# Performance work log

Measured on AMD Instinct MI355X. Metric: run time of the kernel, lower is better.

The kernel has to match this reference:

```python
import jax, jax.numpy as jnp
import numpy as np

B, T, D_MODEL, D_HIDDEN, MAX_SEQLEN = 4, 2048, 1024, 256, 2048


def setup_inputs() -> dict:
    key = jax.random.key(0)
    ks = jax.random.split(key, 8)
    s_in = 1.0 / np.sqrt(D_MODEL)
    s_out = 1.0 / np.sqrt(D_HIDDEN)
    # xavier_uniform bound for W_bias (fan_in = fan_out = MAX_SEQLEN)
    xb = np.sqrt(6.0 / (MAX_SEQLEN + MAX_SEQLEN))
    return {
        "q": jax.random.normal(ks[0], (B, T, D_MODEL), jnp.float32),
        "k": jax.random.normal(ks[1], (B, T, D_MODEL), jnp.float32),
        "v": jax.random.normal(ks[2], (B, T, D_MODEL), jnp.float32),
        "Wq": jax.random.normal(ks[3], (D_MODEL, D_HIDDEN), jnp.float32) * s_in,
        "Wk": jax.random.normal(ks[4], (D_MODEL, D_HIDDEN), jnp.float32) * s_in,
        "Wv": jax.random.normal(ks[5], (D_MODEL, D_HIDDEN), jnp.float32) * s_in,
        "Wo": jax.random.normal(ks[6], (D_HIDDEN, D_MODEL), jnp.float32) * s_out,
        "W_bias": jax.random.uniform(ks[7], (MAX_SEQLEN, MAX_SEQLEN), jnp.float32, -xb, xb),
    }


def reference(q, k, v, Wq, Wk, Wv, Wo, W_bias):
    Ti, Tj = q.shape[1], k.shape[1]
    Q = q @ Wq                      # [B,Ti,dh]
    K = k @ Wk                      # [B,Tj,dh]
    V = v @ Wv                      # [B,Tj,dh]
    pos_bias = W_bias[:Ti, :Tj][None]               # [1,Ti,Tj]
    # NOTE: source subtracts max over dim 0 (batch). For pos_bias that dim is 1,
    # so exp_pos_bias == exp(0) == ones -- reproduced faithfully here.
    max_key = jnp.max(K, axis=0, keepdims=True)      # [1,Tj,dh]
    max_pos_bias = jnp.max(pos_bias, axis=0, keepdims=True)
    exp_key = jnp.exp(K - max_key)                   # [B,Tj,dh]
    exp_pos_bias = jnp.exp(pos_bias - max_pos_bias)  # [1,Ti,Tj]
    num = jnp.einsum('ij,bjd->bid', exp_pos_bias[0], exp_key * V)  # [B,Ti,dh]
    den = jnp.einsum('ij,bjd->bid', exp_pos_bias[0], exp_key)      # [B,Ti,dh]
    Yt = jax.nn.sigmoid(Q) * num / den
    return Yt @ Wo                  # [B,Ti,d_model]
```

## Files before the change

kernel.cpp:

```cpp
#include <hip/hip_runtime.h>
#include <hip/hip_bf16.h>
#include <math.h>

#define B_   4
#define T_   2048
#define DM   1024
#define DH   256
#define M_   (B_*T_)

typedef __bf16 bf16;
typedef __attribute__((ext_vector_type(8))) __bf16 bf16x8;
typedef __attribute__((ext_vector_type(4))) float  f32x4;

#define LDT 72

__device__ inline float sigmoidf_(float x) { return 1.0f / (1.0f + __expf(-x)); }

__global__ void transpose_cvt(const float* __restrict__ in, bf16* __restrict__ out,
                              int R, int C) {
    __shared__ float tile[32][33];
    int c0 = blockIdx.x * 32, r0 = blockIdx.y * 32;
    int tx = threadIdx.x & 31, ty = threadIdx.x >> 5;
    #pragma unroll
    for (int i = ty; i < 32; i += 8)
        tile[i][tx] = in[(long)(r0 + i) * C + c0 + tx];
    __syncthreads();
    #pragma unroll
    for (int i = ty; i < 32; i += 8)
        out[(long)(c0 + i) * R + r0 + tx] = (bf16)tile[tx][i];
}

__global__ __launch_bounds__(256)
void gemm_proj(const float* __restrict__ qin, const float* __restrict__ kin,
               const float* __restrict__ vin,
               const bf16* __restrict__ Wq_t, const bf16* __restrict__ Wk_t,
               const bf16* __restrict__ Wv_t,
               bf16* __restrict__ Qb, bf16* __restrict__ Kb, bf16* __restrict__ Vb)
{
    __shared__ __align__(16) bf16 As[64][LDT];
    __shared__ __align__(16) bf16 Bs[64][LDT];

    const int z = blockIdx.z;
    const float* A  = (z == 0) ? qin  : (z == 1) ? kin  : vin;
    const bf16*  Wt = (z == 0) ? Wq_t : (z == 1) ? Wk_t : Wv_t;
    bf16*        C  = (z == 0) ? Qb   : (z == 1) ? Kb   : Vb;

    const int m0 = blockIdx.x * 64;
    const int n0 = blockIdx.y * 64;
    const int tid = threadIdx.x, lane = tid & 63, wave = tid >> 6;
    const int wr = wave >> 1, wc = wave & 1;
    const int q4 = lane >> 4, l16 = lane & 15;

    f32x4 acc[2][2] = {};
    const int srow = tid >> 3, scol = (tid & 7) * 8;

    for (int k0 = 0; k0 < DM; k0 += 64) {
        #pragma unroll
        for (int h = 0; h < 2; ++h) {
            int row = srow + 32 * h;
            const float* src = &A[(long)(m0 + row) * DM + k0 + scol];
            f32x4 x0 = *(const f32x4*)src;
            f32x4 x1 = *(const f32x4*)(src + 4);
            bf16x8 o;
            #pragma unroll
            for (int e = 0; e < 4; ++e) { o[e] = (bf16)x0[e]; o[4 + e] = (bf16)x1[e]; }
            *(bf16x8*)&As[row][scol] = o;
            *(bf16x8*)&Bs[row][scol] = *(const bf16x8*)&Wt[(long)(n0 + row) * DM + k0 + scol];
        }
        __syncthreads();
        #pragma unroll
        for (int kk = 0; kk < 64; kk += 32) {
            bf16x8 a0 = *(const bf16x8*)&As[wr * 32      + l16][kk + q4 * 8];
            bf16x8 a1 = *(const bf16x8*)&As[wr * 32 + 16 + l16][kk + q4 * 8];
            bf16x8 b0 = *(const bf16x8*)&Bs[wc * 32      + l16][kk + q4 * 8];
            bf16x8 b1 = *(const bf16x8*)&Bs[wc * 32 + 16 + l16][kk + q4 * 8];
            acc[0][0] = __builtin_amdgcn_mfma_f32_16x16x32_bf16(a0, b0, acc[0][0], 0, 0, 0);
            acc[0][1] = __builtin_amdgcn_mfma_f32_16x16x32_bf16(a0, b1, acc[0][1], 0, 0, 0);
            acc[1][0] = __builtin_amdgcn_mfma_f32_16x16x32_bf16(a1, b0, acc[1][0], 0, 0, 0);
            acc[1][1] = __builtin_amdgcn_mfma_f32_16x16x32_bf16(a1, b1, acc[1][1], 0, 0, 0);
        }
        __syncthreads();
    }
    #pragma unroll
    for (int i = 0; i < 2; ++i)
        #pragma unroll
        for (int j = 0; j < 2; ++j)
            #pragma unroll
            for (int r = 0; r < 4; ++r) {
                int gm = m0 + wr * 32 + i * 16 + q4 * 4 + r;
                int gn = n0 + wc * 32 + j * 16 + l16;
                C[(long)gm * DH + gn] = (bf16)acc[i][j][r];
            }
}

__global__ void reduce_kv(const bf16* __restrict__ Kb, const bf16* __restrict__ Vb,
                          float* __restrict__ numb, float* __restrict__ denb)
{
    const int d  = threadIdx.x;
    const int j0 = blockIdx.x * 8;
    float sn[B_] = {0.f, 0.f, 0.f, 0.f};
    float sd[B_] = {0.f, 0.f, 0.f, 0.f};
    for (int jj = 0; jj < 8; ++jj) {
        int j = j0 + jj;
        float kv[B_], vv[B_], mx = -INFINITY;
        #pragma unroll
        for (int b = 0; b < B_; ++b) {
            kv[b] = (float)Kb[((long)b * T_ + j) * DH + d];
            vv[b] = (float)Vb[((long)b * T_ + j) * DH + d];
            mx = fmaxf(mx, kv[b]);
        }
        #pragma unroll
        for (int b = 0; b < B_; ++b) {
            float e = __expf(kv[b] - mx);
            sn[b] += e * vv[b];
            sd[b] += e;
        }
    }
    #pragma unroll
    for (int b = 0; b < B_; ++b) {
        atomicAdd(&numb[b * DH + d], sn[b]);
        atomicAdd(&denb[b * DH + d], sd[b]);
    }
}

__global__ __launch_bounds__(256)
void gemm_out(const bf16* __restrict__ Qb, const bf16* __restrict__ Wo_t,
              const float* __restrict__ numb, const float* __restrict__ denb,
              float* __restrict__ out)
{
    __shared__ __align__(16) bf16 As[64][LDT];
    __shared__ __align__(16) bf16 Bs[64][LDT];

    const int m0 = blockIdx.x * 64;
    const int n0 = blockIdx.y * 64;
    const int b  = blockIdx.x >> 5;
    const int tid = threadIdx.x, lane = tid & 63, wave = tid >> 6;
    const int wr = wave >> 1, wc = wave & 1;
    const int q4 = lane >> 4, l16 = lane & 15;

    f32x4 acc[2][2] = {};
    const int srow = tid >> 3, scol = (tid & 7) * 8;

    for (int k0 = 0; k0 < DH; k0 += 64) {
        f32x4 rn0 = *(const f32x4*)&numb[b * DH + k0 + scol];
        f32x4 rn1 = *(const f32x4*)&numb[b * DH + k0 + scol + 4];
        f32x4 rd0 = *(const f32x4*)&denb[b * DH + k0 + scol];
        f32x4 rd1 = *(const f32x4*)&denb[b * DH + k0 + scol + 4];
        float rv[8];
        #pragma unroll
        for (int e = 0; e < 4; ++e) { rv[e] = rn0[e] / rd0[e]; rv[4 + e] = rn1[e] / rd1[e]; }

        #pragma unroll
        for (int h = 0; h < 2; ++h) {
            int row = srow + 32 * h;
            bf16x8 xq = *(const bf16x8*)&Qb[(long)(m0 + row) * DH + k0 + scol];
            bf16x8 o;
            #pragma unroll
            for (int e = 0; e < 8; ++e)
                o[e] = (bf16)(sigmoidf_((float)xq[e]) * rv[e]);
            *(bf16x8*)&As[row][scol] = o;
            *(bf16x8*)&Bs[row][scol] = *(const bf16x8*)&Wo_t[(long)(n0 + row) * DH + k0 + scol];
        }
        __syncthreads();
        #pragma unroll
        for (int kk = 0; kk < 64; kk += 32) {
            bf16x8 a0 = *(const bf16x8*)&As[wr * 32      + l16][kk + q4 * 8];
            bf16x8 a1 = *(const bf16x8*)&As[wr * 32 + 16 + l16][kk + q4 * 8];
            bf16x8 b0 = *(const bf16x8*)&Bs[wc * 32      + l16][kk + q4 * 8];
            bf16x8 b1 = *(const bf16x8*)&Bs[wc * 32 + 16 + l16][kk + q4 * 8];
            acc[0][0] = __builtin_amdgcn_mfma_f32_16x16x32_bf16(a0, b0, acc[0][0], 0, 0, 0);
            acc[0][1] = __builtin_amdgcn_mfma_f32_16x16x32_bf16(a0, b1, acc[0][1], 0, 0, 0);
            acc[1][0] = __builtin_amdgcn_mfma_f32_16x16x32_bf16(a1, b0, acc[1][0], 0, 0, 0);
            acc[1][1] = __builtin_amdgcn_mfma_f32_16x16x32_bf16(a1, b1, acc[1][1], 0, 0, 0);
        }
        __syncthreads();
    }
    #pragma unroll
    for (int i = 0; i < 2; ++i)
        #pragma unroll
        for (int j = 0; j < 2; ++j)
            #pragma unroll
            for (int r = 0; r < 4; ++r) {
                int gm = m0 + wr * 32 + i * 16 + q4 * 4 + r;
                int gn = n0 + wc * 32 + j * 16 + l16;
                out[(long)gm * DM + gn] = acc[i][j][r];
            }
}

extern "C" void kernel_launch(void* const* d_in, const int* in_sizes, int n_in,
                              void* d_out, int out_size, void* d_ws, size_t ws_size,
                              hipStream_t stream)
{
    const float* q  = (const float*)d_in[0];
    const float* k  = (const float*)d_in[1];
    const float* v  = (const float*)d_in[2];
    const float* Wq = (const float*)d_in[3];
    const float* Wk = (const float*)d_in[4];
    const float* Wv = (const float*)d_in[5];
    const float* Wo = (const float*)d_in[6];
    float* out = (float*)d_out;

    char* ws = (char*)d_ws;
    bf16* Qb    = (bf16*)ws;  ws += (size_t)M_ * DH * sizeof(bf16);
    bf16* Kb    = (bf16*)ws;  ws += (size_t)M_ * DH * sizeof(bf16);
    bf16* Vb    = (bf16*)ws;  ws += (size_t)M_ * DH * sizeof(bf16);
    bf16* Wq_t  = (bf16*)ws;  ws += (size_t)DM * DH * sizeof(bf16);
    bf16* Wk_t  = (bf16*)ws;  ws += (size_t)DM * DH * sizeof(bf16);
    bf16* Wv_t  = (bf16*)ws;  ws += (size_t)DM * DH * sizeof(bf16);
    bf16* Wo_t  = (bf16*)ws;  ws += (size_t)DM * DH * sizeof(bf16);
    float* numb = (float*)ws; ws += (size_t)B_ * DH * sizeof(float);
    float* denb = (float*)ws; ws += (size_t)B_ * DH * sizeof(float);

    transpose_cvt<<<dim3(DH / 32, DM / 32), 256, 0, stream>>>(Wq, Wq_t, DM, DH);
    transpose_cvt<<<dim3(DH / 32, DM / 32), 256, 0, stream>>>(Wk, Wk_t, DM, DH);
    transpose_cvt<<<dim3(DH / 32, DM / 32), 256, 0, stream>>>(Wv, Wv_t, DM, DH);
    transpose_cvt<<<dim3(DM / 32, DH / 32), 256, 0, stream>>>(Wo, Wo_t, DH, DM);

    hipMemsetAsync(numb, 0, 2 * (size_t)B_ * DH * sizeof(float), stream);

    gemm_proj<<<dim3(M_ / 64, DH / 64, 3), 256, 0, stream>>>(q, k, v, Wq_t, Wk_t, Wv_t,
                                                             Qb, Kb, Vb);
    reduce_kv<<<256, 256, 0, stream>>>(Kb, Vb, numb, denb);
    gemm_out<<<dim3(M_ / 64, DM / 64), 256, 0, stream>>>(Qb, Wo_t, numb, denb, out);
}
```

Baseline: 226.3 us.

## Merge weight transposes and memset, widen GEMM tiles, prefetch next K-tile in registers

Folds the four weight transpose launches and the num/den memset into one kernel launch. Both GEMMs now use 512-thread blocks with a 64x128 output tile, so each A tile is reused across twice as many output columns. The next K-slice is prefetched into registers while the MFMAs run on the current one. gemm_out also computes num/den once per block into shared memory instead of redoing the division on every iteration. The cost is higher register and LDS use per block, and half as many blocks in flight.

New measurement: 199.1 us. 1.14x faster.

```diff
diff --git a/kernel.cpp b/kernel.cpp
--- a/kernel.cpp
+++ b/kernel.cpp
@@ -9,6 +9,7 @@
 #define M_   (B_*T_)
 
 typedef __bf16 bf16;
+typedef __attribute__((ext_vector_type(4))) __bf16 bf16x4;
 typedef __attribute__((ext_vector_type(8))) __bf16 bf16x8;
 typedef __attribute__((ext_vector_type(4))) float  f32x4;
 
@@ -16,11 +17,26 @@
 
 __device__ inline float sigmoidf_(float x) { return 1.0f / (1.0f + __expf(-x)); }
 
-__global__ void transpose_cvt(const float* __restrict__ in, bf16* __restrict__ out,
-                              int R, int C) {
+__global__ void transpose_cvt_all(const float* __restrict__ Wq, const float* __restrict__ Wk,
+                                  const float* __restrict__ Wv, const float* __restrict__ Wo,
+                                  bf16* __restrict__ Wq_t, bf16* __restrict__ Wk_t,
+                                  bf16* __restrict__ Wv_t, bf16* __restrict__ Wo_t,
+                                  float* __restrict__ nd)
+{
+    const int bid = blockIdx.x;
+    if (bid >= 1024) {
+        nd[(bid - 1024) * 256 + threadIdx.x] = 0.f;
+        return;
+    }
     __shared__ float tile[32][33];
-    int c0 = blockIdx.x * 32, r0 = blockIdx.y * 32;
-    int tx = threadIdx.x & 31, ty = threadIdx.x >> 5;
+    const int w = bid >> 8, t = bid & 255;
+    const float* in; bf16* out; int R, C, sh;
+    if      (w == 0) { in = Wq; out = Wq_t; R = DM; C = DH; sh = 3; }
+    else if (w == 1) { in = Wk; out = Wk_t; R = DM; C = DH; sh = 3; }
+    else if (w == 2) { in = Wv; out = Wv_t; R = DM; C = DH; sh = 3; }
+    else             { in = Wo; out = Wo_t; R = DH; C = DM; sh = 5; }
+    const int r0 = (t >> sh) * 32, c0 = (t & ((1 << sh) - 1)) * 32;
+    const int tx = threadIdx.x & 31, ty = threadIdx.x >> 5;
     #pragma unroll
     for (int i = ty; i < 32; i += 8)
         tile[i][tx] = in[(long)(r0 + i) * C + c0 + tx];
@@ -30,7 +46,7 @@
         out[(long)(c0 + i) * R + r0 + tx] = (bf16)tile[tx][i];
 }
 
-__global__ __launch_bounds__(256)
+__global__ __launch_bounds__(512, 4)
 void gemm_proj(const float* __restrict__ qin, const float* __restrict__ kin,
                const float* __restrict__ vin,
                const bf16* __restrict__ Wq_t, const bf16* __restrict__ Wk_t,
@@ -38,7 +54,7 @@
                bf16* __restrict__ Qb, bf16* __restrict__ Kb, bf16* __restrict__ Vb)
 {
     __shared__ __align__(16) bf16 As[64][LDT];
-    __shared__ __align__(16) bf16 Bs[64][LDT];
+    __shared__ __align__(16) bf16 Bs[128][LDT];
 
     const int z = blockIdx.z;
     const float* A  = (z == 0) ? qin  : (z == 1) ? kin  : vin;
@@ -46,28 +62,39 @@
     bf16*        C  = (z == 0) ? Qb   : (z == 1) ? Kb   : Vb;
 
     const int m0 = blockIdx.x * 64;
-    const int n0 = blockIdx.y * 64;
+    const int n0 = blockIdx.y * 128;
     const int tid = threadIdx.x, lane = tid & 63, wave = tid >> 6;
-    const int wr = wave >> 1, wc = wave & 1;
+    const int wr = wave >> 2, wc = wave & 3;
     const int q4 = lane >> 4, l16 = lane & 15;
 
     f32x4 acc[2][2] = {};
-    const int srow = tid >> 3, scol = (tid & 7) * 8;
+    const int ar = tid >> 3, ac8 = (tid & 7) * 8;
+    const int br = tid >> 2, bc16 = (tid & 3) * 16;
+
+    f32x4  pa0, pa1;
+    bf16x8 pb0, pb1;
+
+    {   const float* ap = &A[(long)(m0 + ar) * DM + ac8];
+        pa0 = *(const f32x4*)ap; pa1 = *(const f32x4*)(ap + 4);
+        const bf16* bp = &Wt[(long)(n0 + br) * DM + bc16];
+        pb0 = *(const bf16x8*)bp; pb1 = *(const bf16x8*)(bp + 8);
+    }
 
     for (int k0 = 0; k0 < DM; k0 += 64) {
-        #pragma unroll
-        for (int h = 0; h < 2; ++h) {
-            int row = srow + 32 * h;
-            const float* src = &A[(long)(m0 + row) * DM + k0 + scol];
-            f32x4 x0 = *(const f32x4*)src;
-            f32x4 x1 = *(const f32x4*)(src + 4);
-            bf16x8 o;
-            #pragma unroll
-            for (int e = 0; e < 4; ++e) { o[e] = (bf16)x0[e]; o[4 + e] = (bf16)x1[e]; }
-            *(bf16x8*)&As[row][scol] = o;
-            *(bf16x8*)&Bs[row][scol] = *(const bf16x8*)&Wt[(long)(n0 + row) * DM + k0 + scol];
-        }
-        __syncthreads();
+        {   bf16x8 o;
+            #pragma unroll
+            for (int e = 0; e < 4; ++e) { o[e] = (bf16)pa0[e]; o[4 + e] = (bf16)pa1[e]; }
+            *(bf16x8*)&As[ar][ac8] = o;
+            *(bf16x8*)&Bs[br][bc16]     = pb0;
+            *(bf16x8*)&Bs[br][bc16 + 8] = pb1;
+        }
+        __syncthreads();
+        if (k0 + 64 < DM) {
+            const float* ap = &A[(long)(m0 + ar) * DM + k0 + 64 + ac8];
+            pa0 = *(const f32x4*)ap; pa1 = *(const f32x4*)(ap + 4);
+            const bf16* bp = &Wt[(long)(n0 + br) * DM + k0 + 64 + bc16];
+            pb0 = *(const bf16x8*)bp; pb1 = *(const bf16x8*)(bp + 8);
+        }
         #pragma unroll
         for (int kk = 0; kk < 64; kk += 32) {
             bf16x8 a0 = *(const bf16x8*)&As[wr * 32      + l16][kk + q4 * 8];
@@ -123,45 +150,51 @@
     }
 }
 
-__global__ __launch_bounds__(256)
+__global__ __launch_bounds__(512, 4)
 void gemm_out(const bf16* __restrict__ Qb, const bf16* __restrict__ Wo_t,
               const float* __restrict__ numb, const float* __restrict__ denb,
               float* __restrict__ out)
 {
     __shared__ __align__(16) bf16 As[64][LDT];
-    __shared__ __align__(16) bf16 Bs[64][LDT];
+    __shared__ __align__(16) bf16 Bs[128][LDT];
+    __shared__ float rv_s[DH];
 
     const int m0 = blockIdx.x * 64;
-    const int n0 = blockIdx.y * 64;
+    const int n0 = blockIdx.y * 128;
     const int b  = blockIdx.x >> 5;
     const int tid = threadIdx.x, lane = tid & 63, wave = tid >> 6;
-    const int wr = wave >> 1, wc = wave & 1;
+    const int wr = wave >> 2, wc = wave & 3;
     const int q4 = lane >> 4, l16 = lane & 15;
 
+    if (tid < DH) rv_s[tid] = numb[b * DH + tid] / denb[b * DH + tid];
+
     f32x4 acc[2][2] = {};
-    const int srow = tid >> 3, scol = (tid & 7) * 8;
+    const int ar = tid >> 3, ac8 = (tid & 7) * 8;
+    const int br = tid >> 2, bc16 = (tid & 3) * 16;
+
+    bf16x8 pq;
+    bf16x8 pb0, pb1;
+    {   pq  = *(const bf16x8*)&Qb[(long)(m0 + ar) * DH + ac8];
+        const bf16* wp = &Wo_t[(long)(n0 + br) * DH + bc16];
+        pb0 = *(const bf16x8*)wp; pb1 = *(const bf16x8*)(wp + 8);
+    }
+    __syncthreads();
 
     for (int k0 = 0; k0 < DH; k0 += 64) {
-        f32x4 rn0 = *(const f32x4*)&numb[b * DH + k0 + scol];
-        f32x4 rn1 = *(const f32x4*)&numb[b * DH + k0 + scol + 4];
-        f32x4 rd0 = *(const f32x4*)&denb[b * DH + k0 + scol];
-        f32x4 rd1 = *(const f32x4*)&denb[b * DH + k0 + scol + 4];
-        float rv[8];
-        #pragma unroll
-        for (int e = 0; e < 4; ++e) { rv[e] = rn0[e] / rd0[e]; rv[4 + e] = rn1[e] / rd1[e]; }
-
-        #pragma unroll
-        for (int h = 0; h < 2; ++h) {
-            int row = srow + 32 * h;
-            bf16x8 xq = *(const bf16x8*)&Qb[(long)(m0 + row) * DH + k0 + scol];
-            bf16x8 o;
+        {   bf16x8 o;
             #pragma unroll
             for (int e = 0; e < 8; ++e)
-                o[e] = (bf16)(sigmoidf_((float)xq[e]) * rv[e]);
-            *(bf16x8*)&As[row][scol] = o;
-            *(bf16x8*)&Bs[row][scol] = *(const bf16x8*)&Wo_t[(long)(n0 + row) * DH + k0 + scol];
-        }
-        __syncthreads();
+                o[e] = (bf16)(sigmoidf_((float)pq[e]) * rv_s[k0 + ac8 + e]);
+            *(bf16x8*)&As[ar][ac8] = o;
+            *(bf16x8*)&Bs[br][bc16]     = pb0;
+            *(bf16x8*)&Bs[br][bc16 + 8] = pb1;
+        }
+        __syncthreads();
+        if (k0 + 64 < DH) {
+            pq = *(const bf16x8*)&Qb[(long)(m0 + ar) * DH + k0 + 64 + ac8];
+            const bf16* wp = &Wo_t[(long)(n0 + br) * DH + k0 + 64 + bc16];
+            pb0 = *(const bf16x8*)wp; pb1 = *(const bf16x8*)(wp + 8);
+        }
         #pragma unroll
         for (int kk = 0; kk < 64; kk += 32) {
             bf16x8 a0 = *(const bf16x8*)&As[wr * 32      + l16][kk + q4 * 8];
@@ -211,15 +244,11 @@
     float* numb = (float*)ws; ws += (size_t)B_ * DH * sizeof(float);
     float* denb = (float*)ws; ws += (size_t)B_ * DH * sizeof(float);
 
-    transpose_cvt<<<dim3(DH / 32, DM / 32), 256, 0, stream>>>(Wq, Wq_t, DM, DH);
-    transpose_cvt<<<dim3(DH / 32, DM / 32), 256, 0, stream>>>(Wk, Wk_t, DM, DH);
-    transpose_cvt<<<dim3(DH / 32, DM / 32), 256, 0, stream>>>(Wv, Wv_t, DM, DH);
-    transpose_cvt<<<dim3(DM / 32, DH / 32), 256, 0, stream>>>(Wo, Wo_t, DH, DM);
-
-    hipMemsetAsync(numb, 0, 2 * (size_t)B_ * DH * sizeof(float), stream);
-
-    gemm_proj<<<dim3(M_ / 64, DH / 64, 3), 256, 0, stream>>>(q, k, v, Wq_t, Wk_t, Wv_t,
-                                                             Qb, Kb, Vb);
+    transpose_cvt_all<<<1032, 256, 0, stream>>>(Wq, Wk, Wv, Wo,
+                                                Wq_t, Wk_t, Wv_t, Wo_t, numb);
+
+    gemm_proj<<<dim3(M_ / 64, DH / 128, 3), 512, 0, stream>>>(q, k, v, Wq_t, Wk_t, Wv_t,
+                                                              Qb, Kb, Vb);
     reduce_kv<<<256, 256, 0, stream>>>(Kb, Vb, numb, denb);
-    gemm_out<<<dim3(M_ / 64, DM / 64), 256, 0, stream>>>(Qb, Wo_t, numb, denb, out);
-}
+    gemm_out<<<dim3(M_ / 64, DM / 128), 512, 0, stream>>>(Qb, Wo_t, numb, denb, out);
+}
```
